# Performance work log

Measured on AMD Instinct MI355X. Metric: run time of the kernel, lower is better.

## Reference

```python
import jax, jax.numpy as jnp
import numpy as np

N_NODES = 100000
N_EDGES = 1000000
N_LABEL = 200000
D_IN = 64
D_HID = 64


def setup_inputs() -> dict:
    key = jax.random.key(0)
    ks = jax.random.split(key, 9)
    s = 1.0 / np.sqrt(D_IN)
    return {
        "x": jax.random.normal(ks[0], (N_NODES, D_IN), jnp.float32),
        "edge_index": jax.random.randint(ks[1], (2, N_EDGES), 0, N_NODES, jnp.int64),
        "edge_label_index": jax.random.randint(ks[2], (2, N_LABEL), 0, N_NODES, jnp.int64),
        "W1_l": jax.random.normal(ks[3], (D_IN, D_HID), jnp.float32) * s,
        "W1_r": jax.random.normal(ks[4], (D_IN, D_HID), jnp.float32) * s,
        "b1": jnp.zeros((D_HID,), jnp.float32),
        "W2_l": jax.random.normal(ks[5], (D_HID, D_HID), jnp.float32) * s,
        "W2_r": jax.random.normal(ks[6], (D_HID, D_HID), jnp.float32) * s,
        "b2": jnp.zeros((D_HID,), jnp.float32),
    }


def _sage_conv(x, edge_index, W_l, W_r, b):
    # PyG SAGEConv with mean aggregation: out = mean_agg @ W_l + b + x @ W_r
    src, dst = edge_index[0], edge_index[1]
    n = x.shape[0]
    # gather source features, scatter-sum into destination nodes
    agg = jax.ops.segment_sum(x[src], dst, num_segments=n)          # [N, D]
    cnt = jax.ops.segment_sum(jnp.ones(src.shape, x.dtype), dst, num_segments=n)
    mean = agg / jnp.maximum(cnt, 1.0)[:, None]
    return mean @ W_l + x @ W_r + b


def reference(x, edge_index, edge_label_index, W1_l, W1_r, b1, W2_l, W2_r, b2):
    h = jax.nn.relu(_sage_conv(x, edge_index, W1_l, W1_r, b1))
    z = _sage_conv(h, edge_index, W2_l, W2_r, b2)
    # dot-product edge decode
    src_e = z[edge_label_index[0]]  # [E_label, D]
    dst_e = z[edge_label_index[1]]
    return jnp.sum(src_e * dst_e, axis=-1)  # [E_label]
```

## Files before the change

### kernel.cpp

```cpp
#include <hip/hip_runtime.h>

#define D 64
#define NB_SHIFT 9
#define NODES_PER_B 512
#define CAP1 12288

typedef __attribute__((ext_vector_type(8))) short short8;
typedef __attribute__((ext_vector_type(4))) float f32x4;

__device__ inline unsigned short f2bf(float f) {
    unsigned int u = __float_as_uint(f);
    return (unsigned short)((u + 0x7FFFu + ((u >> 16) & 1u)) >> 16);
}
__device__ inline float bf2f(unsigned short s) {
    return __uint_as_float(((unsigned int)s) << 16);
}

__global__ __launch_bounds__(256) void prep_kernel(
        const float* __restrict__ x, unsigned short* __restrict__ xb, int n4,
        const float* __restrict__ W1l, const float* __restrict__ W1r,
        const float* __restrict__ W2l, const float* __restrict__ W2r,
        unsigned short* __restrict__ pw, int* __restrict__ gcount) {
    int gid = blockIdx.x * blockDim.x + threadIdx.x;
    int stride = gridDim.x * blockDim.x;
    for (int t = gid; t < n4; t += stride) {
        float4 v = ((const float4*)x)[t];
        ushort4 o;
        o.x = f2bf(v.x); o.y = f2bf(v.y); o.z = f2bf(v.z); o.w = f2bf(v.w);
        ((ushort4*)xb)[t] = o;
    }
    if (gid < 4 * 4096) {
        int m = gid >> 12;
        int r = gid & 4095;
        const float* W = (m == 0) ? W1l : (m == 1) ? W1r : (m == 2) ? W2l : W2r;
        int j    = r & 7;
        int lane = (r >> 3) & 63;
        int kk   = (r >> 9) & 1;
        int ct   = r >> 10;
        int k    = kk * 32 + ((lane >> 4) & 3) * 8 + j;
        int col  = ct * 16 + (lane & 15);
        pw[gid] = f2bf(W[k * D + col]);
    } else if (gid < 4 * 4096 + 256) {
        gcount[gid - 4 * 4096] = 0;
    }
}

__global__ __launch_bounds__(256) void bin_edges_kernel(
        const int* __restrict__ src, const int* __restrict__ dst,
        int* __restrict__ gcount, int* __restrict__ binned,
        int n_edges, int n_buckets) {
    __shared__ int lhist[256];
    __shared__ int lbase[256];
    int tid = threadIdx.x;
    int per = (((n_edges + gridDim.x - 1) / gridDim.x) + 3) & ~3;
    int beg = blockIdx.x * per;
    int end = min(beg + per, n_edges);
    if (beg >= end) { return; }
    int nv = (end - beg) >> 2;
    const int4* d4p = (const int4*)(dst + beg);
    const int4* s4p = (const int4*)(src + beg);

    lhist[tid] = 0;
    __syncthreads();
    for (int i = tid; i < nv; i += 256) {
        int4 d4 = d4p[i];
        atomicAdd(&lhist[d4.x >> NB_SHIFT], 1);
        atomicAdd(&lhist[d4.y >> NB_SHIFT], 1);
        atomicAdd(&lhist[d4.z >> NB_SHIFT], 1);
        atomicAdd(&lhist[d4.w >> NB_SHIFT], 1);
    }
    for (int e = beg + (nv << 2) + tid; e < end; e += 256)
        atomicAdd(&lhist[dst[e] >> NB_SHIFT], 1);
    __syncthreads();
    if (tid < n_buckets && lhist[tid] > 0)
        lbase[tid] = atomicAdd(&gcount[tid], lhist[tid]);
    else
        lbase[tid] = 0;
    __syncthreads();
    lhist[tid] = 0;
    __syncthreads();
    for (int i = tid; i < nv; i += 256) {
        int4 d4 = d4p[i];
        int4 s4 = s4p[i];
        {
            int b = d4.x >> NB_SHIFT;
            int off = lbase[b] + atomicAdd(&lhist[b], 1);
            if (off < CAP1)
                binned[(size_t)b * CAP1 + off] = (s4.x << NB_SHIFT) | (d4.x & (NODES_PER_B - 1));
        }
        {
            int b = d4.y >> NB_SHIFT;
            int off = lbase[b] + atomicAdd(&lhist[b], 1);
            if (off < CAP1)
                binned[(size_t)b * CAP1 + off] = (s4.y << NB_SHIFT) | (d4.y & (NODES_PER_B - 1));
        }
        {
            int b = d4.z >> NB_SHIFT;
            int off = lbase[b] + atomicAdd(&lhist[b], 1);
            if (off < CAP1)
                binned[(size_t)b * CAP1 + off] = (s4.z << NB_SHIFT) | (d4.z & (NODES_PER_B - 1));
        }
        {
            int b = d4.w >> NB_SHIFT;
            int off = lbase[b] + atomicAdd(&lhist[b], 1);
            if (off < CAP1)
                binned[(size_t)b * CAP1 + off] = (s4.w << NB_SHIFT) | (d4.w & (NODES_PER_B - 1));
        }
    }
    for (int e = beg + (nv << 2) + tid; e < end; e += 256) {
        int d = dst[e];
        int b = d >> NB_SHIFT;
        int off = lbase[b] + atomicAdd(&lhist[b], 1);
        if (off < CAP1)
            binned[(size_t)b * CAP1 + off] = (src[e] << NB_SHIFT) | (d & (NODES_PER_B - 1));
    }
}

__global__ __launch_bounds__(256) void build_csr_kernel(
        const int* __restrict__ binned, const int* __restrict__ gcount,
        int* __restrict__ rowp, int* __restrict__ ssrc,
        int n_nodes, int n_buckets, int n_edges) {
    __shared__ int lhist[NODES_PER_B];
    __shared__ int lbase[NODES_PER_B];
    __shared__ int tmp[256];
    __shared__ int stage[CAP1];

    int b   = blockIdx.x;
    int tid = threadIdx.x;

    int v = (tid < n_buckets) ? min(gcount[tid], CAP1) : 0;
    tmp[tid] = v;
    __syncthreads();
    for (int off = 1; off < 256; off <<= 1) {
        int t = 0;
        if (tid >= off) t = tmp[tid - off];
        __syncthreads();
        if (tid >= off) tmp[tid] += t;
        __syncthreads();
    }
    int base = (b == 0) ? 0 : tmp[b - 1];
    int cnt  = min(gcount[b], CAP1);
    if (b == 0 && tid == 0) rowp[n_nodes] = n_edges;
    __syncthreads();

    int nodebase = b << NB_SHIFT;
    int nlocal   = min(NODES_PER_B, n_nodes - nodebase);
    const int* ebuf = binned + (size_t)b * CAP1;

    lhist[tid] = 0;
    lhist[tid + 256] = 0;
    __syncthreads();
    for (int i = tid; i < cnt; i += 256)
        atomicAdd(&lhist[ebuf[i] & (NODES_PER_B - 1)], 1);
    __syncthreads();

    int a0 = lhist[2 * tid];
    int a1 = lhist[2 * tid + 1];
    tmp[tid] = a0 + a1;
    __syncthreads();
    for (int off = 1; off < 256; off <<= 1) {
        int t = 0;
        if (tid >= off) t = tmp[tid - off];
        __syncthreads();
        if (tid >= off) tmp[tid] += t;
        __syncthreads();
    }
    int excl = tmp[tid] - (a0 + a1);
    lbase[2 * tid]     = excl;
    lbase[2 * tid + 1] = excl + a0;
    __syncthreads();

    for (int j = tid; j < nlocal; j += 256)
        rowp[nodebase + j] = base + lbase[j];

    lhist[tid] = 0;
    lhist[tid + 256] = 0;
    __syncthreads();

    for (int i = tid; i < cnt; i += 256) {
        int e  = ebuf[i];
        int ln = e & (NODES_PER_B - 1);
        int off = atomicAdd(&lhist[ln], 1);
        stage[lbase[ln] + off] = e >> NB_SHIFT;
    }
    __syncthreads();

    for (int i = tid; i < cnt; i += 256)
        ssrc[base + i] = stage[i];
}

__global__ __launch_bounds__(256) void aggregate_bf16_kernel(
        const unsigned short* __restrict__ feat,
        const int* __restrict__ row_ptr,
        const int* __restrict__ sorted_src,
        unsigned short* __restrict__ mean_out,
        int n_nodes) {
    int lane = threadIdx.x & 63;
    int r    = lane >> 4;
    int c    = lane & 15;
    int wave   = (int)((blockIdx.x * blockDim.x + threadIdx.x) >> 6);
    int nwaves = (int)((gridDim.x * blockDim.x) >> 6);
    int npw  = (n_nodes + nwaves - 1) / nwaves;
    int nbeg = wave * npw;
    int nend = min(nbeg + npw, n_nodes);
    if (nbeg >= nend) return;

    int beg = row_ptr[nbeg];
    for (int node = nbeg; node < nend; ++node) {
        int end = row_ptr[node + 1];
        int endm1 = end - 1;
        float a0 = 0.f, a1 = 0.f, a2 = 0.f, a3 = 0.f;

        for (int i = beg; i < end; i += 16) {
            int e0 = i + r, e1 = i + 4 + r, e2 = i + 8 + r, e3 = i + 12 + r;
            int s0 = sorted_src[min(e0, endm1)];
            int s1 = sorted_src[min(e1, endm1)];
            int s2 = sorted_src[min(e2, endm1)];
            int s3 = sorted_src[min(e3, endm1)];
            ushort4 v0 = *(const ushort4*)(feat + ((size_t)s0 << 6) + (c << 2));
            ushort4 v1 = *(const ushort4*)(feat + ((size_t)s1 << 6) + (c << 2));
            ushort4 v2 = *(const ushort4*)(feat + ((size_t)s2 << 6) + (c << 2));
            ushort4 v3 = *(const ushort4*)(feat + ((size_t)s3 << 6) + (c << 2));
            if (e0 < end) {
                a0 += bf2f(v0.x); a1 += bf2f(v0.y);
                a2 += bf2f(v0.z); a3 += bf2f(v0.w);
            }
            if (e1 < end) {
                a0 += bf2f(v1.x); a1 += bf2f(v1.y);
                a2 += bf2f(v1.z); a3 += bf2f(v1.w);
            }
            if (e2 < end) {
                a0 += bf2f(v2.x); a1 += bf2f(v2.y);
                a2 += bf2f(v2.z); a3 += bf2f(v2.w);
            }
            if (e3 < end) {
                a0 += bf2f(v3.x); a1 += bf2f(v3.y);
                a2 += bf2f(v3.z); a3 += bf2f(v3.w);
            }
        }
        a0 += __shfl_xor(a0, 16); a1 += __shfl_xor(a1, 16);
        a2 += __shfl_xor(a2, 16); a3 += __shfl_xor(a3, 16);
        a0 += __shfl_xor(a0, 32); a1 += __shfl_xor(a1, 32);
        a2 += __shfl_xor(a2, 32); a3 += __shfl_xor(a3, 32);

        float inv = 1.0f / (float)max(end - beg, 1);
        if (r == 0) {
            ushort4 o;
            o.x = f2bf(a0 * inv); o.y = f2bf(a1 * inv);
            o.z = f2bf(a2 * inv); o.w = f2bf(a3 * inv);
            *(ushort4*)(mean_out + ((size_t)node << 6) + (c << 2)) = o;
        }
        beg = end;
    }
}

__global__ __launch_bounds__(256) void sage_linear_mfma_kernel(
        const unsigned short* __restrict__ mean,
        const unsigned short* __restrict__ xin,
        const unsigned short* __restrict__ pwl,
        const unsigned short* __restrict__ pwr,
        const float* __restrict__ bias,
        unsigned short* __restrict__ outp,
        int n_nodes, int do_relu) {
    int lane = threadIdx.x & 63;
    int wid  = threadIdx.x >> 6;
    int arow = lane & 15;
    int kgrp = lane >> 4;

    short8 wl[4][2], wr[4][2];
#pragma unroll
    for (int ct = 0; ct < 4; ++ct)
#pragma unroll
        for (int kk = 0; kk < 2; ++kk) {
            wl[ct][kk] = *(const short8*)(pwl + (((ct * 2 + kk) * 64 + lane) << 3));
            wr[ct][kk] = *(const short8*)(pwr + (((ct * 2 + kk) * 64 + lane) << 3));
        }
    float bj[4];
#pragma unroll
    for (int ct = 0; ct < 4; ++ct) bj[ct] = bias[ct * 16 + arow];

    int wave   = blockIdx.x * 4 + wid;
    int nwaves = gridDim.x * 4;
    int ntiles = (n_nodes + 15) >> 4;

    for (int t = wave; t < ntiles; t += nwaves) {
        int base = t * 16;
        int lrow = base + arow;
        if (lrow >= n_nodes) lrow = n_nodes - 1;
        const unsigned short* mrow = mean + (size_t)lrow * D + kgrp * 8;
        const unsigned short* xrow = xin  + (size_t)lrow * D + kgrp * 8;
        short8 am0 = *(const short8*)(mrow);
        short8 am1 = *(const short8*)(mrow + 32);
        short8 ax0 = *(const short8*)(xrow);
        short8 ax1 = *(const short8*)(xrow + 32);

#pragma unroll
        for (int ct = 0; ct < 4; ++ct) {
            f32x4 acc = {0.f, 0.f, 0.f, 0.f};
            acc = __builtin_amdgcn_mfma_f32_16x16x32_bf16(am0, wl[ct][0], acc, 0, 0, 0);
            acc = __builtin_amdgcn_mfma_f32_16x16x32_bf16(am1, wl[ct][1], acc, 0, 0, 0);
            acc = __builtin_amdgcn_mfma_f32_16x16x32_bf16(ax0, wr[ct][0], acc, 0, 0, 0);
            acc = __builtin_amdgcn_mfma_f32_16x16x32_bf16(ax1, wr[ct][1], acc, 0, 0, 0);
            int col = ct * 16 + arow;
#pragma unroll
            for (int rr = 0; rr < 4; ++rr) {
                int row = base + kgrp * 4 + rr;
                float v = acc[rr] + bj[ct];
                if (do_relu) v = fmaxf(v, 0.0f);
                if (row < n_nodes) outp[(size_t)row * D + col] = f2bf(v);
            }
        }
    }
}

__global__ __launch_bounds__(256) void decode_bf16_kernel(
        const unsigned short* __restrict__ z,
        const int* __restrict__ esrc,
        const int* __restrict__ edst,
        float* __restrict__ out,
        int n) {
    int lane = threadIdx.x & 63;
    int g    = lane >> 4;
    int c    = lane & 15;
    int wave   = (int)((blockIdx.x * blockDim.x + threadIdx.x) >> 6);
    int nwaves = (int)((gridDim.x * blockDim.x) >> 6);
    int niter  = (n + 7) >> 3;

    for (int it = wave; it < niter; it += nwaves) {
        int e0 = it * 8 + g;
        int e1 = it * 8 + 4 + g;
        int ec0 = min(e0, n - 1);
        int ec1 = min(e1, n - 1);
        int s0  = esrc[ec0], d0 = edst[ec0];
        int s1  = esrc[ec1], d1 = edst[ec1];
        ushort4 vs0 = *(const ushort4*)(z + ((size_t)s0 << 6) + (c << 2));
        ushort4 vd0 = *(const ushort4*)(z + ((size_t)d0 << 6) + (c << 2));
        ushort4 vs1 = *(const ushort4*)(z + ((size_t)s1 << 6) + (c << 2));
        ushort4 vd1 = *(const ushort4*)(z + ((size_t)d1 << 6) + (c << 2));
        float p0 = bf2f(vs0.x) * bf2f(vd0.x) + bf2f(vs0.y) * bf2f(vd0.y) +
                   bf2f(vs0.z) * bf2f(vd0.z) + bf2f(vs0.w) * bf2f(vd0.w);
        float p1 = bf2f(vs1.x) * bf2f(vd1.x) + bf2f(vs1.y) * bf2f(vd1.y) +
                   bf2f(vs1.z) * bf2f(vd1.z) + bf2f(vs1.w) * bf2f(vd1.w);
        p0 += __shfl_xor(p0, 1);  p1 += __shfl_xor(p1, 1);
        p0 += __shfl_xor(p0, 2);  p1 += __shfl_xor(p1, 2);
        p0 += __shfl_xor(p0, 4);  p1 += __shfl_xor(p1, 4);
        p0 += __shfl_xor(p0, 8);  p1 += __shfl_xor(p1, 8);
        if (c == 0 && e0 < n) out[e0] = p0;
        if (c == 0 && e1 < n) out[e1] = p1;
    }
}

extern "C" void kernel_launch(void* const* d_in, const int* in_sizes, int n_in,
                              void* d_out, int out_size, void* d_ws, size_t ws_size,
                              hipStream_t stream) {
    const float* x   = (const float*)d_in[0];
    const int*   ei  = (const int*)d_in[1];
    const int*   eli = (const int*)d_in[2];
    const float* W1l = (const float*)d_in[3];
    const float* W1r = (const float*)d_in[4];
    const float* b1  = (const float*)d_in[5];
    const float* W2l = (const float*)d_in[6];
    const float* W2r = (const float*)d_in[7];
    const float* b2  = (const float*)d_in[8];
    float* out = (float*)d_out;

    const int n_nodes = in_sizes[0] / D;
    const int n_edges = in_sizes[1] / 2;
    const int n_label = in_sizes[2] / 2;
    const int n_buckets = (n_nodes + NODES_PER_B - 1) >> NB_SHIFT;

    const int* e_src = ei;
    const int* e_dst = ei + n_edges;
    const int* l_src = eli;
    const int* l_dst = eli + n_label;

    unsigned short* xb    = (unsigned short*)d_ws;
    unsigned short* meanb = xb + (size_t)n_nodes * D;
    unsigned short* h     = meanb + (size_t)n_nodes * D;
    unsigned short* z     = h + (size_t)n_nodes * D;
    int* rowp   = (int*)(z + (size_t)n_nodes * D);
    int* ssrc   = rowp + (n_nodes + 1);
    int* gcount = ssrc + n_edges + 8;
    unsigned short* pw = (unsigned short*)(gcount + 256);
    unsigned short* pw1l = pw;
    unsigned short* pw1r = pw + 4096;
    unsigned short* pw2l = pw + 8192;
    unsigned short* pw2r = pw + 12288;
    int* binned = (int*)h;

    dim3 blk(256);
    dim3 grd_nodes(2048);
    dim3 grd_linear(782);

    prep_kernel<<<dim3(2048), blk, 0, stream>>>(x, xb, n_nodes * D / 4,
                                                W1l, W1r, W2l, W2r, pw, gcount);

    bin_edges_kernel<<<dim3(512), blk, 0, stream>>>(e_src, e_dst, gcount, binned,
                                                    n_edges, n_buckets);
    build_csr_kernel<<<dim3(n_buckets), blk, 0, stream>>>(binned, gcount, rowp,
                                                          ssrc, n_nodes,
                                                          n_buckets, n_edges);

    aggregate_bf16_kernel<<<grd_nodes, blk, 0, stream>>>(xb, rowp, ssrc, meanb, n_nodes);
    sage_linear_mfma_kernel<<<grd_linear, blk, 0, stream>>>(meanb, xb, pw1l, pw1r, b1,
                                                            h, n_nodes, 1);

    aggregate_bf16_kernel<<<grd_nodes, blk, 0, stream>>>(h, rowp, ssrc, meanb, n_nodes);
    sage_linear_mfma_kernel<<<grd_linear, blk, 0, stream>>>(meanb, h, pw2l, pw2r, b2,
                                                            z, n_nodes, 0);

    decode_bf16_kernel<<<dim3(2048), blk, 0, stream>>>(z, l_src, l_dst, out, n_label);
}
```

Baseline: 136.5 us.

## Fuse prep and edge binning into one launch; aggregate two nodes per wave

Merges the bf16 conversion/weight packing kernel with the edge binning kernel into a single launch by partitioning block indices, and moves the gcount zeroing to a hipMemsetAsync. The aggregation kernel now processes two destination nodes per iteration, issuing all index and feature loads for both up front when both degrees are at most 16, so more gathers are in flight per wave. This removes one kernel launch and one serialization point and raises memory-level parallelism in aggregation, at the cost of more registers and an extra memset call.

```diff
diff --git a/kernel.cpp b/kernel.cpp
--- a/kernel.cpp
+++ b/kernel.cpp
@@ -4,6 +4,7 @@
 #define NB_SHIFT 9
 #define NODES_PER_B 512
 #define CAP1 12288
+#define NBIN_BLOCKS 512
 
 typedef __attribute__((ext_vector_type(8))) short short8;
 typedef __attribute__((ext_vector_type(4))) float f32x4;
@@ -16,46 +17,51 @@
     return __uint_as_float(((unsigned int)s) << 16);
 }
 
-__global__ __launch_bounds__(256) void prep_kernel(
+__global__ __launch_bounds__(256) void prep_bin_kernel(
+        const int* __restrict__ src, const int* __restrict__ dst,
+        int* __restrict__ gcount, int* __restrict__ binned,
+        int n_edges, int n_buckets,
         const float* __restrict__ x, unsigned short* __restrict__ xb, int n4,
         const float* __restrict__ W1l, const float* __restrict__ W1r,
         const float* __restrict__ W2l, const float* __restrict__ W2r,
-        unsigned short* __restrict__ pw, int* __restrict__ gcount) {
-    int gid = blockIdx.x * blockDim.x + threadIdx.x;
-    int stride = gridDim.x * blockDim.x;
-    for (int t = gid; t < n4; t += stride) {
-        float4 v = ((const float4*)x)[t];
-        ushort4 o;
-        o.x = f2bf(v.x); o.y = f2bf(v.y); o.z = f2bf(v.z); o.w = f2bf(v.w);
-        ((ushort4*)xb)[t] = o;
-    }
-    if (gid < 4 * 4096) {
-        int m = gid >> 12;
-        int r = gid & 4095;
-        const float* W = (m == 0) ? W1l : (m == 1) ? W1r : (m == 2) ? W2l : W2r;
-        int j    = r & 7;
-        int lane = (r >> 3) & 63;
-        int kk   = (r >> 9) & 1;
-        int ct   = r >> 10;
-        int k    = kk * 32 + ((lane >> 4) & 3) * 8 + j;
-        int col  = ct * 16 + (lane & 15);
-        pw[gid] = f2bf(W[k * D + col]);
-    } else if (gid < 4 * 4096 + 256) {
-        gcount[gid - 4 * 4096] = 0;
-    }
-}
-
-__global__ __launch_bounds__(256) void bin_edges_kernel(
-        const int* __restrict__ src, const int* __restrict__ dst,
-        int* __restrict__ gcount, int* __restrict__ binned,
-        int n_edges, int n_buckets) {
+        unsigned short* __restrict__ pw) {
+    int blk = blockIdx.x;
+    int tid = threadIdx.x;
+
+    if (blk >= NBIN_BLOCKS) {
+        if (blk < 2 * NBIN_BLOCKS) {
+            int gid = (blk - NBIN_BLOCKS) * 256 + tid;
+            int stride = NBIN_BLOCKS * 256;
+            for (int t = gid; t < n4; t += stride) {
+                float4 v = ((const float4*)x)[t];
+                ushort4 o;
+                o.x = f2bf(v.x); o.y = f2bf(v.y); o.z = f2bf(v.z); o.w = f2bf(v.w);
+                ((ushort4*)xb)[t] = o;
+            }
+        } else {
+            int idx = (blk - 2 * NBIN_BLOCKS) * 256 + tid;
+            if (idx < 4 * 4096) {
+                int m = idx >> 12;
+                int r = idx & 4095;
+                const float* W = (m == 0) ? W1l : (m == 1) ? W1r : (m == 2) ? W2l : W2r;
+                int j    = r & 7;
+                int lane = (r >> 3) & 63;
+                int kk   = (r >> 9) & 1;
+                int ct   = r >> 10;
+                int k    = kk * 32 + ((lane >> 4) & 3) * 8 + j;
+                int col  = ct * 16 + (lane & 15);
+                pw[idx] = f2bf(W[k * D + col]);
+            }
+        }
+        return;
+    }
+
     __shared__ int lhist[256];
     __shared__ int lbase[256];
-    int tid = threadIdx.x;
-    int per = (((n_edges + gridDim.x - 1) / gridDim.x) + 3) & ~3;
-    int beg = blockIdx.x * per;
+    int per = (((n_edges + NBIN_BLOCKS - 1) / NBIN_BLOCKS) + 3) & ~3;
+    int beg = blk * per;
     int end = min(beg + per, n_edges);
-    if (beg >= end) { return; }
+    if (beg >= end) return;
     int nv = (end - beg) >> 2;
     const int4* d4p = (const int4*)(dst + beg);
     const int4* s4p = (const int4*)(src + beg);
@@ -206,51 +212,104 @@
     if (nbeg >= nend) return;
 
     int beg = row_ptr[nbeg];
-    for (int node = nbeg; node < nend; ++node) {
-        int end = row_ptr[node + 1];
-        int endm1 = end - 1;
+    for (int node = nbeg; node < nend; node += 2) {
+        bool two = (node + 1 < nend);
+        int end0 = row_ptr[node + 1];
+        int end1 = two ? row_ptr[node + 2] : end0;
+        int beg0 = beg, beg1 = end0;
+        int d0 = end0 - beg0, d1 = end1 - beg1;
         float a0 = 0.f, a1 = 0.f, a2 = 0.f, a3 = 0.f;
-
-        for (int i = beg; i < end; i += 16) {
-            int e0 = i + r, e1 = i + 4 + r, e2 = i + 8 + r, e3 = i + 12 + r;
-            int s0 = sorted_src[min(e0, endm1)];
-            int s1 = sorted_src[min(e1, endm1)];
-            int s2 = sorted_src[min(e2, endm1)];
-            int s3 = sorted_src[min(e3, endm1)];
-            ushort4 v0 = *(const ushort4*)(feat + ((size_t)s0 << 6) + (c << 2));
-            ushort4 v1 = *(const ushort4*)(feat + ((size_t)s1 << 6) + (c << 2));
-            ushort4 v2 = *(const ushort4*)(feat + ((size_t)s2 << 6) + (c << 2));
-            ushort4 v3 = *(const ushort4*)(feat + ((size_t)s3 << 6) + (c << 2));
-            if (e0 < end) {
-                a0 += bf2f(v0.x); a1 += bf2f(v0.y);
-                a2 += bf2f(v0.z); a3 += bf2f(v0.w);
-            }
-            if (e1 < end) {
-                a0 += bf2f(v1.x); a1 += bf2f(v1.y);
-                a2 += bf2f(v1.z); a3 += bf2f(v1.w);
-            }
-            if (e2 < end) {
-                a0 += bf2f(v2.x); a1 += bf2f(v2.y);
-                a2 += bf2f(v2.z); a3 += bf2f(v2.w);
-            }
-            if (e3 < end) {
-                a0 += bf2f(v3.x); a1 += bf2f(v3.y);
-                a2 += bf2f(v3.z); a3 += bf2f(v3.w);
-            }
-        }
+        float b0 = 0.f, b1 = 0.f, b2 = 0.f, b3 = 0.f;
+
+        if (d0 <= 16 && d1 <= 16) {
+            int em0 = end0 - 1, em1 = end1 - 1;
+            int ea0 = beg0 + r,     ea1 = beg0 + 4 + r;
+            int ea2 = beg0 + 8 + r, ea3 = beg0 + 12 + r;
+            int eb0 = beg1 + r,     eb1 = beg1 + 4 + r;
+            int eb2 = beg1 + 8 + r, eb3 = beg1 + 12 + r;
+            int sa0 = sorted_src[max(min(ea0, em0), 0)];
+            int sa1 = sorted_src[max(min(ea1, em0), 0)];
+            int sa2 = sorted_src[max(min(ea2, em0), 0)];
+            int sa3 = sorted_src[max(min(ea3, em0), 0)];
+            int sb0 = sorted_src[max(min(eb0, em1), 0)];
+            int sb1 = sorted_src[max(min(eb1, em1), 0)];
+            int sb2 = sorted_src[max(min(eb2, em1), 0)];
+            int sb3 = sorted_src[max(min(eb3, em1), 0)];
+            ushort4 va0 = *(const ushort4*)(feat + ((size_t)sa0 << 6) + (c << 2));
+            ushort4 va1 = *(const ushort4*)(feat + ((size_t)sa1 << 6) + (c << 2));
+            ushort4 va2 = *(const ushort4*)(feat + ((size_t)sa2 << 6) + (c << 2));
+            ushort4 va3 = *(const ushort4*)(feat + ((size_t)sa3 << 6) + (c << 2));
+            ushort4 vb0 = *(const ushort4*)(feat + ((size_t)sb0 << 6) + (c << 2));
+            ushort4 vb1 = *(const ushort4*)(feat + ((size_t)sb1 << 6) + (c << 2));
+            ushort4 vb2 = *(const ushort4*)(feat + ((size_t)sb2 << 6) + (c << 2));
+            ushort4 vb3 = *(const ushort4*)(feat + ((size_t)sb3 << 6) + (c << 2));
+            if (ea0 < end0) { a0 += bf2f(va0.x); a1 += bf2f(va0.y); a2 += bf2f(va0.z); a3 += bf2f(va0.w); }
+            if (ea1 < end0) { a0 += bf2f(va1.x); a1 += bf2f(va1.y); a2 += bf2f(va1.z); a3 += bf2f(va1.w); }
+            if (ea2 < end0) { a0 += bf2f(va2.x); a1 += bf2f(va2.y); a2 += bf2f(va2.z); a3 += bf2f(va2.w); }
+            if (ea3 < end0) { a0 += bf2f(va3.x); a1 += bf2f(va3.y); a2 += bf2f(va3.z); a3 += bf2f(va3.w); }
+            if (eb0 < end1) { b0 += bf2f(vb0.x); b1 += bf2f(vb0.y); b2 += bf2f(vb0.z); b3 += bf2f(vb0.w); }
+            if (eb1 < end1) { b0 += bf2f(vb1.x); b1 += bf2f(vb1.y); b2 += bf2f(vb1.z); b3 += bf2f(vb1.w); }
+            if (eb2 < end1) { b0 += bf2f(vb2.x); b1 += bf2f(vb2.y); b2 += bf2f(vb2.z); b3 += bf2f(vb2.w); }
+            if (eb3 < end1) { b0 += bf2f(vb3.x); b1 += bf2f(vb3.y); b2 += bf2f(vb3.z); b3 += bf2f(vb3.w); }
+        } else {
+            int em0 = end0 - 1;
+            for (int i = beg0; i < end0; i += 16) {
+                int e0 = i + r, e1 = i + 4 + r, e2 = i + 8 + r, e3 = i + 12 + r;
+                int s0 = sorted_src[min(e0, em0)];
+                int s1 = sorted_src[min(e1, em0)];
+                int s2 = sorted_src[min(e2, em0)];
+                int s3 = sorted_src[min(e3, em0)];
+                ushort4 v0 = *(const ushort4*)(feat + ((size_t)s0 << 6) + (c << 2));
+                ushort4 v1 = *(const ushort4*)(feat + ((size_t)s1 << 6) + (c << 2));
+                ushort4 v2 = *(const ushort4*)(feat + ((size_t)s2 << 6) + (c << 2));
+                ushort4 v3 = *(const ushort4*)(feat + ((size_t)s3 << 6) + (c << 2));
+                if (e0 < end0) { a0 += bf2f(v0.x); a1 += bf2f(v0.y); a2 += bf2f(v0.z); a3 += bf2f(v0.w); }
+                if (e1 < end0) { a0 += bf2f(v1.x); a1 += bf2f(v1.y); a2 += bf2f(v1.z); a3 += bf2f(v1.w); }
+                if (e2 < end0) { a0 += bf2f(v2.x); a1 += bf2f(v2.y); a2 += bf2f(v2.z); a3 += bf2f(v2.w); }
+                if (e3 < end0) { a0 += bf2f(v3.x); a1 += bf2f(v3.y); a2 += bf2f(v3.z); a3 += bf2f(v3.w); }
+            }
+            int em1 = end1 - 1;
+            for (int i = beg1; i < end1; i += 16) {
+                int e0 = i + r, e1 = i + 4 + r, e2 = i + 8 + r, e3 = i + 12 + r;
+                int s0 = sorted_src[min(e0, em1)];
+                int s1 = sorted_src[min(e1, em1)];
+                int s2 = sorted_src[min(e2, em1)];
+                int s3 = sorted_src[min(e3, em1)];
+                ushort4 v0 = *(const ushort4*)(feat + ((size_t)s0 << 6) + (c << 2));
+                ushort4 v1 = *(const ushort4*)(feat + ((size_t)s1 << 6) + (c << 2));
+                ushort4 v2 = *(const ushort4*)(feat + ((size_t)s2 << 6) + (c << 2));
+                ushort4 v3 = *(const ushort4*)(feat + ((size_t)s3 << 6) + (c << 2));
+                if (e0 < end1) { b0 += bf2f(v0.x); b1 += bf2f(v0.y); b2 += bf2f(v0.z); b3 += bf2f(v0.w); }
+                if (e1 < end1) { b0 += bf2f(v1.x); b1 += bf2f(v1.y); b2 += bf2f(v1.z); b3 += bf2f(v1.w); }
+                if (e2 < end1) { b0 += bf2f(v2.x); b1 += bf2f(v2.y); b2 += bf2f(v2.z); b3 += bf2f(v2.w); }
+                if (e3 < end1) { b0 += bf2f(v3.x); b1 += bf2f(v3.y); b2 += bf2f(v3.z); b3 += bf2f(v3.w); }
+            }
+        }
+
         a0 += __shfl_xor(a0, 16); a1 += __shfl_xor(a1, 16);
         a2 += __shfl_xor(a2, 16); a3 += __shfl_xor(a3, 16);
         a0 += __shfl_xor(a0, 32); a1 += __shfl_xor(a1, 32);
         a2 += __shfl_xor(a2, 32); a3 += __shfl_xor(a3, 32);
-
-        float inv = 1.0f / (float)max(end - beg, 1);
+        b0 += __shfl_xor(b0, 16); b1 += __shfl_xor(b1, 16);
+        b2 += __shfl_xor(b2, 16); b3 += __shfl_xor(b3, 16);
+        b0 += __shfl_xor(b0, 32); b1 += __shfl_xor(b1, 32);
+        b2 += __shfl_xor(b2, 32); b3 += __shfl_xor(b3, 32);
+
         if (r == 0) {
+            float inv0 = 1.0f / (float)max(d0, 1);
             ushort4 o;
-            o.x = f2bf(a0 * inv); o.y = f2bf(a1 * inv);
-            o.z = f2bf(a2 * inv); o.w = f2bf(a3 * inv);
+            o.x = f2bf(a0 * inv0); o.y = f2bf(a1 * inv0);
+            o.z = f2bf(a2 * inv0); o.w = f2bf(a3 * inv0);
             *(ushort4*)(mean_out + ((size_t)node << 6) + (c << 2)) = o;
-        }
-        beg = end;
+            if (two) {
+                float inv1 = 1.0f / (float)max(d1, 1);
+                ushort4 p;
+                p.x = f2bf(b0 * inv1); p.y = f2bf(b1 * inv1);
+                p.z = f2bf(b2 * inv1); p.w = f2bf(b3 * inv1);
+                *(ushort4*)(mean_out + ((size_t)(node + 1) << 6) + (c << 2)) = p;
+            }
+        }
+        beg = end1;
     }
 }
 
@@ -391,12 +450,13 @@
     dim3 blk(256);
     dim3 grd_nodes(2048);
     dim3 grd_linear(782);
-
-    prep_kernel<<<dim3(2048), blk, 0, stream>>>(x, xb, n_nodes * D / 4,
-                                                W1l, W1r, W2l, W2r, pw, gcount);
-
-    bin_edges_kernel<<<dim3(512), blk, 0, stream>>>(e_src, e_dst, gcount, binned,
-                                                    n_edges, n_buckets);
+    dim3 grd_prepbin(2 * NBIN_BLOCKS + 64);
+
+    hipMemsetAsync(gcount, 0, 256 * sizeof(int), stream);
+    prep_bin_kernel<<<grd_prepbin, blk, 0, stream>>>(
+        e_src, e_dst, gcount, binned, n_edges, n_buckets,
+        x, xb, n_nodes * D / 4, W1l, W1r, W2l, W2r, pw);
+
     build_csr_kernel<<<dim3(n_buckets), blk, 0, stream>>>(binned, gcount, rowp,
                                                           ssrc, n_nodes,
                                                           n_buckets, n_edges);
```

New measurement: 142.3 us. 4.3% more time.
